# Optimization experiments

Measured on AMD Instinct MI355X. Metric: run time of the kernel, lower is better.

Reference implementation:

```python
import jax, jax.numpy as jnp
import numpy as np

SHAPES = ((496, 432), (248, 216), (124, 108))
NS = (40000, 20000, 8000)
T = 32
B = 4
EPS = 1e-3


def _bn(x, g, b, m, v):
    return (x - m) * (g / jnp.sqrt(v + EPS)) + b


def _vfe_scale(voxels, num_pts, w1, p1, w2, p2):
    # voxels: (N, T, 4); num_pts: (N,)
    Tp = voxels.shape[1]
    n = num_pts.astype(voxels.dtype)[:, None, None]
    m3 = voxels[:, :, :3].sum(axis=1, keepdims=True) / n
    m2 = voxels[:, :, :2].sum(axis=1, keepdims=True) / n
    feat = jnp.concatenate([voxels[:, :, :4], voxels[:, :, :3] - m3, voxels[:, :, :2] - m2], axis=-1)  # (N,T,9)
    mask = (jnp.arange(Tp)[None, :] < num_pts[:, None]).astype(voxels.dtype)[:, :, None]
    x = feat
    for w, (g, b_, rm, rv) in ((w1, p1), (w2, p2)):
        h = jax.nn.relu(_bn(jnp.einsum('ntc,cd->ntd', x, w), g, b_, rm, rv))  # (N,T,64)
        gmax = h.max(axis=1, keepdims=True)  # global max includes padded rows, as in torch source
        x = jnp.concatenate([h, jnp.broadcast_to(gmax, h.shape)], axis=-1) * mask  # (N,T,128)
    return x.max(axis=1)[:, :64]  # (N,64)


def _scatter_bev(vf, coords, h, w, batch_size):
    b = coords[:, 0]
    y = jnp.clip(coords[:, 2], 0, h - 1)
    x = jnp.clip(coords[:, 3], 0, w - 1)
    grid = jnp.zeros((batch_size, vf.shape[1], h, w), vf.dtype)
    return grid.at[b, :, y, x].set(vf)


def _fusion(x, w, g, b, m, v):
    y = jax.lax.conv_general_dilated(x, w, (1, 1), ((1, 1), (1, 1)),
                                     dimension_numbers=('NCHW', 'OIHW', 'NCHW'))
    y = _bn(y, g[None, :, None, None], b[None, :, None, None], m[None, :, None, None], v[None, :, None, None])
    return jax.nn.relu(y)


def setup_inputs() -> dict:
    key = jax.random.key(0)
    ks = jax.random.split(key, 32)
    inp = {}
    for s in range(3):
        h, w = SHAPES[s]
        inp[f'voxels_{s}'] = jax.random.normal(ks[s], (NS[s], T, 4), dtype=jnp.float32)
        inp[f'num_pts_{s}'] = jax.random.randint(ks[3 + s], (NS[s],), 1, T + 1, dtype=jnp.int32)
        b = jax.random.randint(ks[6 + s], (NS[s],), 0, B, dtype=jnp.int32)
        z = jnp.zeros((NS[s],), jnp.int32)
        y = jax.random.randint(ks[9 + s], (NS[s],), 0, h, dtype=jnp.int32)
        x = jax.random.randint(ks[12 + s], (NS[s],), 0, w, dtype=jnp.int32)
        inp[f'coords_{s}'] = jnp.stack([b, z, y, x], axis=1)
    # VFE params (stacked across the 3 scales; identical shapes per scale)
    inp['w1'] = jax.random.normal(ks[15], (3, 9, 64), dtype=jnp.float32) * 0.1
    inp['g1'] = jnp.ones((3, 64), jnp.float32) + 0.1 * jax.random.normal(ks[16], (3, 64))
    inp['b1'] = 0.05 * jax.random.normal(ks[17], (3, 64))
    inp['rm1'] = 0.05 * jax.random.normal(ks[18], (3, 64))
    inp['rv1'] = 0.5 + jnp.abs(jax.random.normal(ks[19], (3, 64)))
    inp['w2'] = jax.random.normal(ks[20], (3, 128, 64), dtype=jnp.float32) * 0.05
    inp['g2'] = jnp.ones((3, 64), jnp.float32) + 0.1 * jax.random.normal(ks[21], (3, 64))
    inp['b2'] = 0.05 * jax.random.normal(ks[22], (3, 64))
    inp['rm2'] = 0.05 * jax.random.normal(ks[23], (3, 64))
    inp['rv2'] = 0.5 + jnp.abs(jax.random.normal(ks[24], (3, 64)))
    # Fusion convs (2): Conv2d(128,64,3) + BN
    inp['fw'] = jax.random.normal(ks[25], (2, 64, 128, 3, 3), dtype=jnp.float32) * 0.03
    inp['fg'] = jnp.ones((2, 64), jnp.float32) + 0.1 * jax.random.normal(ks[26], (2, 64))
    inp['fb'] = 0.05 * jax.random.normal(ks[27], (2, 64))
    inp['fm'] = 0.05 * jax.random.normal(ks[28], (2, 64))
    inp['fv'] = 0.5 + jnp.abs(jax.random.normal(ks[29], (2, 64)))
    inp['batch_size'] = B
    return inp


def reference(voxels_0, voxels_1, voxels_2,
              w1, g1, b1, rm1, rv1, w2, g2, b2, rm2, rv2,
              fw, fg, fb, fm, fv,
              num_pts_0, num_pts_1, num_pts_2,
              coords_0, coords_1, coords_2, batch_size):
    voxels = (voxels_0, voxels_1, voxels_2)
    num_pts = (num_pts_0, num_pts_1, num_pts_2)
    coords = (coords_0, coords_1, coords_2)
    sf = []
    for s in range(3):
        vf = _vfe_scale(voxels[s], num_pts[s],
                        w1[s], (g1[s], b1[s], rm1[s], rv1[s]),
                        w2[s], (g2[s], b2[s], rm2[s], rv2[s]))
        h, w = SHAPES[s]
        sf.append(_scatter_bev(vf, coords[s], h, w, batch_size))
    # bottom-up fusion: scale2 -> scale1 -> scale0
    up = jax.image.resize(sf[2], sf[1].shape[:2] + SHAPES[1], method='bilinear')
    fused_1 = _fusion(jnp.concatenate([sf[1], up], axis=1), fw[1], fg[1], fb[1], fm[1], fv[1])
    up = jax.image.resize(fused_1, fused_1.shape[:2] + SHAPES[0], method='bilinear')
    fused_0 = _fusion(jnp.concatenate([sf[0], up], axis=1), fw[0], fg[0], fb[0], fm[0], fv[0])
    return fused_0  # spatial_features_2d: (B, 64, 496, 432)
```

## Files before the change

### kernel.cpp

```cpp
#include <hip/hip_runtime.h>

typedef unsigned short u16;
typedef short bf16x8 __attribute__((ext_vector_type(8)));
typedef float f32x4 __attribute__((ext_vector_type(4)));

#define EPSV 1e-3f

__device__ __forceinline__ float bf2f(u16 u) {
  union { unsigned int i; float f; } x; x.i = ((unsigned int)u) << 16; return x.f;
}
__device__ __forceinline__ u16 f2bf(float f) {
  union { float f; unsigned int i; } x; x.f = f;
  unsigned int r = x.i + 0x7fffu + ((x.i >> 16) & 1u);
  return (u16)(r >> 16);
}

#define WAVE_FENCE() do { __builtin_amdgcn_s_waitcnt(0); __builtin_amdgcn_wave_barrier(); } while (0)

__global__ void twt_kernel(const float* __restrict__ fw, u16* __restrict__ fwT) {
  int i = blockIdx.x * blockDim.x + threadIdx.x;
  if (i >= 2 * 9 * 64 * 128) return;
  int ci = i & 127;
  int r = i >> 7;
  int co = r & 63; r >>= 6;
  int kyx = r % 9;
  int set = r / 9;
  fwT[i] = f2bf(fw[(((set * 64 + co) * 128 + ci) * 9) + kyx]);
}

__global__ __launch_bounds__(256, 2) void vfe_mfma_kernel(
    const float* __restrict__ vox, const int* __restrict__ npts,
    const float* __restrict__ w1, const float* __restrict__ g1, const float* __restrict__ b1,
    const float* __restrict__ rm1, const float* __restrict__ rv1,
    const float* __restrict__ w2, const float* __restrict__ g2, const float* __restrict__ b2,
    const float* __restrict__ rm2, const float* __restrict__ rv2,
    float* __restrict__ vf, int N)
{
  struct PerWave {
    u16 X[32 * 72];
    u16 F[32 * 40];
    u16 G[64];
  };
  __shared__ __align__(16) union {
    struct { u16 W1T[64 * 40]; u16 W2T[64 * 136]; } w;
    PerWave r[4];
  } lds;

  const int tid = threadIdx.x;
  const int lane = tid & 63;
  const int wv = tid >> 6;
  const int m16 = lane & 15;
  const int q = lane >> 4;

  for (int i = tid; i < 64 * 40; i += 256) {
    int c = i / 40, k = i % 40;
    lds.w.W1T[i] = f2bf(k < 9 ? w1[k * 64 + c] : 0.f);
  }
  for (int i = tid; i < 64 * 136; i += 256) {
    int c = i / 136, j = i % 136;
    lds.w.W2T[i] = f2bf(j < 128 ? w2[j * 64 + c] : 0.f);
  }
  __syncthreads();

  bf16x8 bW1[4], bLo[4][2], bHi[4][2];
  float sc1[4], sh1[4], sc2[4], sh2[4];
#pragma unroll
  for (int nf = 0; nf < 4; ++nf) {
    int c = nf * 16 + m16;
    bW1[nf] = *(const bf16x8*)&lds.w.W1T[c * 40 + q * 8];
#pragma unroll
    for (int ks = 0; ks < 2; ++ks) {
      bLo[nf][ks] = *(const bf16x8*)&lds.w.W2T[c * 136 + ks * 32 + q * 8];
      bHi[nf][ks] = *(const bf16x8*)&lds.w.W2T[c * 136 + 64 + ks * 32 + q * 8];
    }
    float s1 = g1[c] * rsqrtf(rv1[c] + EPSV);
    sc1[nf] = s1; sh1[nf] = b1[c] - rm1[c] * s1;
    float s2 = g2[c] * rsqrtf(rv2[c] + EPSV);
    sc2[nf] = s2; sh2[nf] = b2[c] - rm2[c] * s2;
  }
  __syncthreads();

  u16* X = lds.r[wv].X;
  u16* F = lds.r[wv].F;
  u16* G = lds.r[wv].G;
  for (int i = lane; i < 640; i += 64) ((unsigned int*)F)[i] = 0u;

  const int wgid = blockIdx.x * 4 + wv;
  const int wstride = gridDim.x * 4;

  for (int v = wgid; v < N; v += wstride) {
    const int n = npts[v];
    float px = 0.f, py = 0.f, pz = 0.f, pw = 0.f;
    if (lane < 32) {
      float4 u = *(const float4*)(vox + ((size_t)v * 32 + lane) * 4);
      px = u.x; py = u.y; pz = u.z; pw = u.w;
    }
    float sx = px, sy = py, sz = pz;
#pragma unroll
    for (int off = 32; off >= 1; off >>= 1) {
      sx += __shfl_xor(sx, off);
      sy += __shfl_xor(sy, off);
      sz += __shfl_xor(sz, off);
    }
    float nf_ = (float)n;
    float mx = sx / nf_, my = sy / nf_, mz = sz / nf_;
    if (lane < 32) {
      float dx = px - mx, dy = py - my, dz = pz - mz;
      bf16x8 r0, r1;
      r0[0] = (short)f2bf(px); r0[1] = (short)f2bf(py);
      r0[2] = (short)f2bf(pz); r0[3] = (short)f2bf(pw);
      r0[4] = (short)f2bf(dx); r0[5] = (short)f2bf(dy);
      r0[6] = (short)f2bf(dz); r0[7] = (short)f2bf(dx);
      r1 = (bf16x8){0, 0, 0, 0, 0, 0, 0, 0};
      r1[0] = (short)f2bf(dy);
      *(bf16x8*)&F[lane * 40 + 0] = r0;
      *(bf16x8*)&F[lane * 40 + 8] = r1;
    }
    WAVE_FENCE();

    bf16x8 a1[2];
    a1[0] = *(const bf16x8*)&F[m16 * 40 + q * 8];
    a1[1] = *(const bf16x8*)&F[(16 + m16) * 40 + q * 8];
    f32x4 acc1[2][4];
#pragma unroll
    for (int mf = 0; mf < 2; ++mf)
#pragma unroll
      for (int nf = 0; nf < 4; ++nf) {
        acc1[mf][nf] = (f32x4){0.f, 0.f, 0.f, 0.f};
        acc1[mf][nf] = __builtin_amdgcn_mfma_f32_16x16x32_bf16(a1[mf], bW1[nf], acc1[mf][nf], 0, 0, 0);
      }

    float gmx[4] = {0.f, 0.f, 0.f, 0.f};
#pragma unroll
    for (int mf = 0; mf < 2; ++mf)
#pragma unroll
      for (int nf = 0; nf < 4; ++nf)
#pragma unroll
        for (int r = 0; r < 4; ++r) {
          float h = fmaxf(acc1[mf][nf][r] * sc1[nf] + sh1[nf], 0.f);
          gmx[nf] = fmaxf(gmx[nf], h);
          int t = mf * 16 + q * 4 + r;
          X[t * 72 + nf * 16 + m16] = f2bf(h);
        }
#pragma unroll
    for (int nf = 0; nf < 4; ++nf) {
      gmx[nf] = fmaxf(gmx[nf], __shfl_xor(gmx[nf], 16));
      gmx[nf] = fmaxf(gmx[nf], __shfl_xor(gmx[nf], 32));
    }
    if (q == 0) {
#pragma unroll
      for (int nf = 0; nf < 4; ++nf) G[nf * 16 + m16] = f2bf(gmx[nf]);
    }
    WAVE_FENCE();

    f32x4 ga[4];
#pragma unroll
    for (int nf = 0; nf < 4; ++nf) ga[nf] = (f32x4){0.f, 0.f, 0.f, 0.f};
#pragma unroll
    for (int ks = 0; ks < 2; ++ks) {
      bf16x8 ag = (bf16x8){0, 0, 0, 0, 0, 0, 0, 0};
      if (m16 == 0) ag = *(const bf16x8*)&G[ks * 32 + q * 8];
#pragma unroll
      for (int nf = 0; nf < 4; ++nf)
        ga[nf] = __builtin_amdgcn_mfma_f32_16x16x32_bf16(ag, bHi[nf][ks], ga[nf], 0, 0, 0);
    }
    float gt[4];
#pragma unroll
    for (int nf = 0; nf < 4; ++nf) {
      float s = ga[nf][0] + ga[nf][1] + ga[nf][2] + ga[nf][3];
      s += __shfl_xor(s, 16);
      s += __shfl_xor(s, 32);
      gt[nf] = s;
    }

    f32x4 acc2[2][4];
#pragma unroll
    for (int mf = 0; mf < 2; ++mf)
#pragma unroll
      for (int nf = 0; nf < 4; ++nf)
        acc2[mf][nf] = (f32x4){gt[nf], gt[nf], gt[nf], gt[nf]};
#pragma unroll
    for (int ks = 0; ks < 2; ++ks) {
      bf16x8 a2[2];
      a2[0] = *(const bf16x8*)&X[m16 * 72 + ks * 32 + q * 8];
      a2[1] = *(const bf16x8*)&X[(16 + m16) * 72 + ks * 32 + q * 8];
#pragma unroll
      for (int mf = 0; mf < 2; ++mf)
#pragma unroll
        for (int nf = 0; nf < 4; ++nf)
          acc2[mf][nf] = __builtin_amdgcn_mfma_f32_16x16x32_bf16(a2[mf], bLo[nf][ks], acc2[mf][nf], 0, 0, 0);
    }

    float vm[4] = {0.f, 0.f, 0.f, 0.f};
#pragma unroll
    for (int mf = 0; mf < 2; ++mf)
#pragma unroll
      for (int nf = 0; nf < 4; ++nf)
#pragma unroll
        for (int r = 0; r < 4; ++r) {
          int t = mf * 16 + q * 4 + r;
          float h2 = fmaxf(acc2[mf][nf][r] * sc2[nf] + sh2[nf], 0.f);
          if (t < n) vm[nf] = fmaxf(vm[nf], h2);
        }
#pragma unroll
    for (int nf = 0; nf < 4; ++nf) {
      vm[nf] = fmaxf(vm[nf], __shfl_xor(vm[nf], 16));
      vm[nf] = fmaxf(vm[nf], __shfl_xor(vm[nf], 32));
    }
    float outv = (q == 0) ? vm[0] : (q == 1) ? vm[1] : (q == 2) ? vm[2] : vm[3];
    vf[(size_t)v * 64 + q * 16 + m16] = outv;
    __builtin_amdgcn_wave_barrier();
  }
}

__global__ void winner_kernel(const int* __restrict__ coords, int* __restrict__ win,
                              int N, int H, int W) {
  int v = blockIdx.x * blockDim.x + threadIdx.x;
  if (v >= N) return;
  int b = coords[v * 4 + 0];
  int y = min(max(coords[v * 4 + 2], 0), H - 1);
  int x = min(max(coords[v * 4 + 3], 0), W - 1);
  atomicMax(&win[(b * H + y) * W + x], v);
}

__global__ void fill_kernel(const int* __restrict__ win, const float* __restrict__ vf,
                            u16* __restrict__ dst, int cells, int cstride) {
  int i = blockIdx.x * blockDim.x + threadIdx.x;
  if (i >= cells * 8) return;
  int cell = i >> 3, c8 = (i & 7) * 8;
  int wv = win[cell];
  bf16x8 o = (bf16x8){0, 0, 0, 0, 0, 0, 0, 0};
  if (wv >= 0) {
    const float* p = vf + (size_t)wv * 64 + c8;
    float4 v0 = *(const float4*)p;
    float4 v1 = *(const float4*)(p + 4);
    o[0] = (short)f2bf(v0.x); o[1] = (short)f2bf(v0.y);
    o[2] = (short)f2bf(v0.z); o[3] = (short)f2bf(v0.w);
    o[4] = (short)f2bf(v1.x); o[5] = (short)f2bf(v1.y);
    o[6] = (short)f2bf(v1.z); o[7] = (short)f2bf(v1.w);
  }
  *(bf16x8*)&dst[(size_t)cell * cstride + c8] = o;
}

__global__ void upsample_kernel(const u16* __restrict__ src, u16* __restrict__ dst,
                                int Hc, int Wc, int dstride, int doff, int total8) {
  int i = blockIdx.x * blockDim.x + threadIdx.x;
  if (i >= total8) return;
  int c8 = (i & 7) * 8;
  int px = i >> 3;
  int W2 = Wc * 2, H2 = Hc * 2;
  int x = px % W2; int t = px / W2; int y = t % H2; int n = t / H2;
  int ky = y >> 1, kx = x >> 1;
  int ya, yb, xa, xb; float wya, wxa;
  if ((y & 1) == 0) { ya = ky > 0 ? ky - 1 : 0; yb = ky; wya = 0.25f; }
  else              { ya = ky; yb = (ky + 1 < Hc) ? ky + 1 : Hc - 1; wya = 0.75f; }
  if ((x & 1) == 0) { xa = kx > 0 ? kx - 1 : 0; xb = kx; wxa = 0.25f; }
  else              { xa = kx; xb = (kx + 1 < Wc) ? kx + 1 : Wc - 1; wxa = 0.75f; }
  float wyb = 1.f - wya, wxb = 1.f - wxa;
  const u16* sp = src + c8;
  bf16x8 vaa = *(const bf16x8*)&sp[((size_t)(n * Hc + ya) * Wc + xa) * 64];
  bf16x8 vab = *(const bf16x8*)&sp[((size_t)(n * Hc + ya) * Wc + xb) * 64];
  bf16x8 vba = *(const bf16x8*)&sp[((size_t)(n * Hc + yb) * Wc + xa) * 64];
  bf16x8 vbb = *(const bf16x8*)&sp[((size_t)(n * Hc + yb) * Wc + xb) * 64];
  bf16x8 o;
#pragma unroll
  for (int j = 0; j < 8; ++j) {
    float v = wya * (wxa * bf2f((u16)vaa[j]) + wxb * bf2f((u16)vab[j])) +
              wyb * (wxa * bf2f((u16)vba[j]) + wxb * bf2f((u16)vbb[j]));
    o[j] = (short)f2bf(v);
  }
  *(bf16x8*)&dst[(size_t)px * dstride + doff + c8] = o;
}

template<int H, int W, bool NCHW_OUT>
__global__ __launch_bounds__(256, 2) void conv_kernel(
    const u16* __restrict__ in, const u16* __restrict__ wT,
    const float* __restrict__ fg, const float* __restrict__ fb,
    const float* __restrict__ fm, const float* __restrict__ fv,
    void* __restrict__ outv)
{
  constexpr int XT = 24, YT = 8;
  constexpr int XTILES = W / XT;
  constexpr int NPX = 10 * 26;
  __shared__ __align__(16) union {
    struct { char A[NPX * 128]; char B[2][8192]; } s;
    float T[4 * 64 * 33];
  } lds;

  const int tid = threadIdx.x;
  const int lane = tid & 63;
  const int wv = tid >> 6;
  const int m16 = lane & 15;
  const int q = lane >> 4;

  int bid = blockIdx.x;
  const int xt = bid % XTILES; bid /= XTILES;
  const int yt = bid % (H / YT);
  const int n = bid / (H / YT);
  const int x0 = xt * XT, y0 = yt * YT;

  int lin[3];
#pragma unroll
  for (int mf = 0; mf < 3; ++mf) {
    int m = mf * 16 + m16;
    int r = (m >= 24) ? 1 : 0;
    lin[mf] = (2 * wv + r) * 26 + (m - r * 24);
  }
  const int qb = q * 16;
  const int bsw = (m16 & 7) << 4;

  f32x4 acc[3][4];
#pragma unroll
  for (int mf = 0; mf < 3; ++mf)
#pragma unroll
    for (int nf = 0; nf < 4; ++nf)
      acc[mf][nf] = (f32x4){0.f, 0.f, 0.f, 0.f};

  for (int hf = 0; hf < 2; ++hf) {
    {
      const int slot = tid & 7;
      const int cis = slot * 8;
      const int pb = tid >> 3;
#pragma unroll
      for (int it = 0; it < 9; ++it) {
        int p = pb + it * 32;
        if (p < NPX) {
          int r = p / 26, xx = p - r * 26;
          int gy = y0 - 1 + r, gx = x0 - 1 + xx;
          uint4 v = make_uint4(0, 0, 0, 0);
          if (gy >= 0 && gy < H && gx >= 0 && gx < W)
            v = *(const uint4*)(in + ((size_t)((n * H + gy) * W + gx) * 128 + hf * 64 + cis));
          *(uint4*)(lds.s.A + p * 128 + ((slot << 4) ^ ((p & 7) << 4))) = v;
        }
      }
#pragma unroll
      for (int it = 0; it < 2; ++it) {
        int e = it * 256 + tid;
        int co = e >> 3, bs = e & 7;
        uint4 v = *(const uint4*)(wT + hf * 64 + co * 128 + bs * 8);
        *(uint4*)(lds.s.B[0] + co * 128 + ((bs << 4) ^ ((co & 7) << 4))) = v;
      }
    }
    __syncthreads();

#pragma unroll
    for (int kyx = 0; kyx < 9; ++kyx) {
      uint4 bv0, bv1;
      if (kyx < 8) {
        const u16* ws = wT + (kyx + 1) * 8192 + hf * 64;
        int co0 = tid >> 3, bs0 = tid & 7;
        bv0 = *(const uint4*)(ws + co0 * 128 + bs0 * 8);
        int e1 = 256 + tid;
        int co1 = e1 >> 3, bs1 = e1 & 7;
        bv1 = *(const uint4*)(ws + co1 * 128 + bs1 * 8);
      }
      const int tapofs = (kyx / 3) * 26 + (kyx % 3);
      const char* Bb = lds.s.B[kyx & 1];
#pragma unroll
      for (int cc = 0; cc < 2; ++cc) {
        const int o = cc * 64 + qb;
        bf16x8 b[4], a[3];
#pragma unroll
        for (int nf = 0; nf < 4; ++nf)
          b[nf] = *(const bf16x8*)(Bb + nf * 2048 + m16 * 128 + (o ^ bsw));
#pragma unroll
        for (int mf = 0; mf < 3; ++mf) {
          int p = lin[mf] + tapofs;
          a[mf] = *(const bf16x8*)(lds.s.A + p * 128 + (o ^ ((p & 7) << 4)));
        }
#pragma unroll
        for (int mf = 0; mf < 3; ++mf)
#pragma unroll
          for (int nf = 0; nf < 4; ++nf)
            acc[mf][nf] = __builtin_amdgcn_mfma_f32_16x16x32_bf16(a[mf], b[nf], acc[mf][nf], 0, 0, 0);
      }
      if (kyx < 8) {
        char* Bw = lds.s.B[(kyx + 1) & 1];
        int co0 = tid >> 3, bs0 = tid & 7;
        *(uint4*)(Bw + co0 * 128 + ((bs0 << 4) ^ ((co0 & 7) << 4))) = bv0;
        int e1 = 256 + tid;
        int co1 = e1 >> 3, bs1 = e1 & 7;
        *(uint4*)(Bw + co1 * 128 + ((bs1 << 4) ^ ((co1 & 7) << 4))) = bv1;
      }
      __syncthreads();
    }
  }

  float sc[4], sh[4];
#pragma unroll
  for (int nf = 0; nf < 4; ++nf) {
    int co = nf * 16 + m16;
    float s = fg[co] * rsqrtf(fv[co] + EPSV);
    sc[nf] = s;
    sh[nf] = fb[co] - fm[co] * s;
  }

  if (!NCHW_OUT) {
    u16* out = (u16*)outv;
#pragma unroll
    for (int mf = 0; mf < 3; ++mf)
#pragma unroll
      for (int nf = 0; nf < 4; ++nf)
#pragma unroll
        for (int r = 0; r < 4; ++r) {
          int mpos = mf * 16 + q * 4 + r;
          int rr = (mpos >= 24) ? 1 : 0;
          int px = mpos - rr * 24;
          int y = y0 + wv * 2 + rr;
          int x = x0 + px;
          int co = nf * 16 + m16;
          float v = fmaxf(acc[mf][nf][r] * sc[nf] + sh[nf], 0.f);
          out[((size_t)(n * H + y) * W + x) * 64 + co] = f2bf(v);
        }
  } else {
    __syncthreads();
    float* out = (float*)outv;
    float* T = &lds.T[wv * 64 * 33];
#pragma unroll
    for (int rr = 0; rr < 2; ++rr) {
#pragma unroll
      for (int mf = 0; mf < 3; ++mf)
#pragma unroll
        for (int nf = 0; nf < 4; ++nf)
#pragma unroll
          for (int r = 0; r < 4; ++r) {
            int mpos = mf * 16 + q * 4 + r;
            if ((mpos >= 24 ? 1 : 0) == rr) {
              int px = mpos - rr * 24;
              int co = nf * 16 + m16;
              T[co * 33 + px] = fmaxf(acc[mf][nf][r] * sc[nf] + sh[nf], 0.f);
            }
          }
      WAVE_FENCE();
      const int px = lane & 31, co2 = lane >> 5;
      const int y = y0 + wv * 2 + rr;
      int x = x0 + px;
#pragma unroll 4
      for (int it = 0; it < 32; ++it) {
        int co = it * 2 + co2;
        float v = T[co * 33 + px];
        if (px < 24) out[((size_t)(n * 64 + co) * H + y) * W + x] = v;
      }
      WAVE_FENCE();
    }
  }
}

extern "C" void kernel_launch(void* const* d_in, const int* in_sizes, int n_in,
                              void* d_out, int out_size, void* d_ws, size_t ws_size,
                              hipStream_t stream) {
  int I_vox[3], I_np[3], I_co[3];
  int I_w1, I_g1, I_b1, I_rm1, I_rv1, I_w2, I_g2, I_b2, I_rm2, I_rv2;
  int I_fw, I_fg, I_fb, I_fm, I_fv;
  if (in_sizes[1] == 40000) {
    I_vox[0] = 0; I_np[0] = 1; I_co[0] = 2;
    I_vox[1] = 3; I_np[1] = 4; I_co[1] = 5;
    I_vox[2] = 6; I_np[2] = 7; I_co[2] = 8;
    I_w1 = 9; I_g1 = 10; I_b1 = 11; I_rm1 = 12; I_rv1 = 13;
    I_w2 = 14; I_g2 = 15; I_b2 = 16; I_rm2 = 17; I_rv2 = 18;
    I_fw = 19; I_fg = 20; I_fb = 21; I_fm = 22; I_fv = 23;
  } else {
    I_vox[0] = 0; I_vox[1] = 1; I_vox[2] = 2;
    I_w1 = 3; I_g1 = 4; I_b1 = 5; I_rm1 = 6; I_rv1 = 7;
    I_w2 = 8; I_g2 = 9; I_b2 = 10; I_rm2 = 11; I_rv2 = 12;
    I_fw = 13; I_fg = 14; I_fb = 15; I_fm = 16; I_fv = 17;
    I_np[0] = 18; I_np[1] = 19; I_np[2] = 20;
    I_co[0] = 21; I_co[1] = 22; I_co[2] = 23;
  }

  const int HS[3] = {496, 248, 124};
  const int WS[3] = {432, 216, 108};
  int Nv[3];
  for (int s = 0; s < 3; ++s) Nv[s] = in_sizes[I_np[s]];

  char* wsp = (char*)d_ws;
  size_t off = 0;
  auto take = [&](size_t bytes) -> void* {
    void* p = wsp + off;
    off = (off + bytes + 255) & ~(size_t)255;
    return p;
  };
  float* vf[3]; int* win[3];
  for (int s = 0; s < 3; ++s) vf[s] = (float*)take((size_t)Nv[s] * 64 * 4);
  int cells[3];
  for (int s = 0; s < 3; ++s) {
    cells[s] = 4 * HS[s] * WS[s];
    win[s] = (int*)take((size_t)cells[s] * 4);
  }
  u16* buf0 = (u16*)take((size_t)cells[0] * 128 * 2);
  u16* buf1 = (u16*)take((size_t)cells[1] * 128 * 2);
  u16* g2b  = (u16*)take((size_t)cells[2] * 64 * 2);
  u16* fus1 = (u16*)take((size_t)cells[1] * 64 * 2);
  u16* fwT  = (u16*)take((size_t)2 * 9 * 64 * 128 * 2);

  const float* W1 = (const float*)d_in[I_w1];
  const float* G1 = (const float*)d_in[I_g1];
  const float* B1 = (const float*)d_in[I_b1];
  const float* RM1 = (const float*)d_in[I_rm1];
  const float* RV1 = (const float*)d_in[I_rv1];
  const float* W2 = (const float*)d_in[I_w2];
  const float* G2 = (const float*)d_in[I_g2];
  const float* B2 = (const float*)d_in[I_b2];
  const float* RM2 = (const float*)d_in[I_rm2];
  const float* RV2 = (const float*)d_in[I_rv2];
  const float* FW = (const float*)d_in[I_fw];
  const float* FG = (const float*)d_in[I_fg];
  const float* FB = (const float*)d_in[I_fb];
  const float* FM = (const float*)d_in[I_fm];
  const float* FV = (const float*)d_in[I_fv];

  for (int s = 0; s < 3; ++s)
    hipMemsetAsync(win[s], 0xFF, (size_t)cells[s] * 4, stream);

  twt_kernel<<<(2 * 9 * 64 * 128 + 255) / 256, 256, 0, stream>>>(FW, fwT);

  for (int s = 0; s < 3; ++s) {
    int blocks = (Nv[s] + 3) / 4;
    if (blocks > 1024) blocks = 1024;
    vfe_mfma_kernel<<<blocks, 256, 0, stream>>>(
        (const float*)d_in[I_vox[s]], (const int*)d_in[I_np[s]],
        W1 + s * 9 * 64, G1 + s * 64, B1 + s * 64, RM1 + s * 64, RV1 + s * 64,
        W2 + s * 128 * 64, G2 + s * 64, B2 + s * 64, RM2 + s * 64, RV2 + s * 64,
        vf[s], Nv[s]);
  }
  for (int s = 0; s < 3; ++s) {
    winner_kernel<<<(Nv[s] + 255) / 256, 256, 0, stream>>>(
        (const int*)d_in[I_co[s]], win[s], Nv[s], HS[s], WS[s]);
  }
  fill_kernel<<<(cells[0] * 8 + 255) / 256, 256, 0, stream>>>(win[0], vf[0], buf0, cells[0], 128);
  fill_kernel<<<(cells[1] * 8 + 255) / 256, 256, 0, stream>>>(win[1], vf[1], buf1, cells[1], 128);
  fill_kernel<<<(cells[2] * 8 + 255) / 256, 256, 0, stream>>>(win[2], vf[2], g2b, cells[2], 64);

  {
    int total8 = cells[1] * 8;
    upsample_kernel<<<(total8 + 255) / 256, 256, 0, stream>>>(g2b, buf1, 124, 108, 128, 64, total8);
  }
  conv_kernel<248, 216, false><<<4 * (248 / 8) * (216 / 24), 256, 0, stream>>>(
      buf1, fwT + 9 * 64 * 128, FG + 64, FB + 64, FM + 64, FV + 64, fus1);
  {
    int total8 = cells[0] * 8;
    upsample_kernel<<<(total8 + 255) / 256, 256, 0, stream>>>(fus1, buf0, 248, 216, 128, 64, total8);
  }
  conv_kernel<496, 432, true><<<4 * (496 / 8) * (432 / 24), 256, 0, stream>>>(
      buf0, fwT, FG, FB, FM, FV, (float*)d_out);
}
```

Baseline: 831.6 us.

## Widen conv tile to 32 columns with four M fragments and edge masking

The conv tile width grows from 24 to 32 pixels, so each wave computes four 16-row MFMA fragments instead of three. Each B-weight fragment load is then reused across more A fragments, and the halo overhead per output pixel shrinks. Widths that are not multiples of 32 (216, 432) need partial tiles, which wastes some compute on masked columns and adds bounds checks. LDS use and accumulator register pressure also rise.

```diff
diff --git a/kernel.cpp b/kernel.cpp
--- a/kernel.cpp
+++ b/kernel.cpp
@@ -279,9 +279,9 @@
     const float* __restrict__ fm, const float* __restrict__ fv,
     void* __restrict__ outv)
 {
-  constexpr int XT = 24, YT = 8;
-  constexpr int XTILES = W / XT;
-  constexpr int NPX = 10 * 26;
+  constexpr int XT = 32, YT = 8;
+  constexpr int XTILES = (W + XT - 1) / XT;
+  constexpr int NPX = 10 * 34;
   __shared__ __align__(16) union {
     struct { char A[NPX * 128]; char B[2][8192]; } s;
     float T[4 * 64 * 33];
@@ -299,19 +299,18 @@
   const int n = bid / (H / YT);
   const int x0 = xt * XT, y0 = yt * YT;
 
-  int lin[3];
-#pragma unroll
-  for (int mf = 0; mf < 3; ++mf) {
+  int lin[4];
+#pragma unroll
+  for (int mf = 0; mf < 4; ++mf) {
     int m = mf * 16 + m16;
-    int r = (m >= 24) ? 1 : 0;
-    lin[mf] = (2 * wv + r) * 26 + (m - r * 24);
+    lin[mf] = (2 * wv + (m >> 5)) * 34 + (m & 31);
   }
   const int qb = q * 16;
   const int bsw = (m16 & 7) << 4;
 
-  f32x4 acc[3][4];
-#pragma unroll
-  for (int mf = 0; mf < 3; ++mf)
+  f32x4 acc[4][4];
+#pragma unroll
+  for (int mf = 0; mf < 4; ++mf)
 #pragma unroll
     for (int nf = 0; nf < 4; ++nf)
       acc[mf][nf] = (f32x4){0.f, 0.f, 0.f, 0.f};
@@ -322,10 +321,10 @@
       const int cis = slot * 8;
       const int pb = tid >> 3;
 #pragma unroll
-      for (int it = 0; it < 9; ++it) {
+      for (int it = 0; it < 11; ++it) {
         int p = pb + it * 32;
         if (p < NPX) {
-          int r = p / 26, xx = p - r * 26;
+          int r = p / 34, xx = p - r * 34;
           int gy = y0 - 1 + r, gx = x0 - 1 + xx;
           uint4 v = make_uint4(0, 0, 0, 0);
           if (gy >= 0 && gy < H && gx >= 0 && gx < W)
@@ -354,22 +353,22 @@
         int co1 = e1 >> 3, bs1 = e1 & 7;
         bv1 = *(const uint4*)(ws + co1 * 128 + bs1 * 8);
       }
-      const int tapofs = (kyx / 3) * 26 + (kyx % 3);
+      const int tapofs = (kyx / 3) * 34 + (kyx % 3);
       const char* Bb = lds.s.B[kyx & 1];
 #pragma unroll
       for (int cc = 0; cc < 2; ++cc) {
         const int o = cc * 64 + qb;
-        bf16x8 b[4], a[3];
+        bf16x8 b[4], a[4];
 #pragma unroll
         for (int nf = 0; nf < 4; ++nf)
           b[nf] = *(const bf16x8*)(Bb + nf * 2048 + m16 * 128 + (o ^ bsw));
 #pragma unroll
-        for (int mf = 0; mf < 3; ++mf) {
+        for (int mf = 0; mf < 4; ++mf) {
           int p = lin[mf] + tapofs;
           a[mf] = *(const bf16x8*)(lds.s.A + p * 128 + (o ^ ((p & 7) << 4)));
         }
 #pragma unroll
-        for (int mf = 0; mf < 3; ++mf)
+        for (int mf = 0; mf < 4; ++mf)
 #pragma unroll
           for (int nf = 0; nf < 4; ++nf)
             acc[mf][nf] = __builtin_amdgcn_mfma_f32_16x16x32_bf16(a[mf], b[nf], acc[mf][nf], 0, 0, 0);
@@ -398,48 +397,46 @@
   if (!NCHW_OUT) {
     u16* out = (u16*)outv;
 #pragma unroll
-    for (int mf = 0; mf < 3; ++mf)
+    for (int mf = 0; mf < 4; ++mf) {
+      int y = y0 + wv * 2 + (mf >> 1);
 #pragma unroll
       for (int nf = 0; nf < 4; ++nf)
 #pragma unroll
         for (int r = 0; r < 4; ++r) {
-          int mpos = mf * 16 + q * 4 + r;
-          int rr = (mpos >= 24) ? 1 : 0;
-          int px = mpos - rr * 24;
-          int y = y0 + wv * 2 + rr;
+          int px = (mf & 1) * 16 + q * 4 + r;
           int x = x0 + px;
-          int co = nf * 16 + m16;
-          float v = fmaxf(acc[mf][nf][r] * sc[nf] + sh[nf], 0.f);
-          out[((size_t)(n * H + y) * W + x) * 64 + co] = f2bf(v);
+          if (x < W) {
+            int co = nf * 16 + m16;
+            float v = fmaxf(acc[mf][nf][r] * sc[nf] + sh[nf], 0.f);
+            out[((size_t)(n * H + y) * W + x) * 64 + co] = f2bf(v);
+          }
         }
+    }
   } else {
     __syncthreads();
     float* out = (float*)outv;
     float* T = &lds.T[wv * 64 * 33];
 #pragma unroll
-    for (int rr = 0; rr < 2; ++rr) {
-#pragma unroll
-      for (int mf = 0; mf < 3; ++mf)
+    for (int yr = 0; yr < 2; ++yr) {
+#pragma unroll
+      for (int xc = 0; xc < 2; ++xc)
 #pragma unroll
         for (int nf = 0; nf < 4; ++nf)
 #pragma unroll
           for (int r = 0; r < 4; ++r) {
-            int mpos = mf * 16 + q * 4 + r;
-            if ((mpos >= 24 ? 1 : 0) == rr) {
-              int px = mpos - rr * 24;
-              int co = nf * 16 + m16;
-              T[co * 33 + px] = fmaxf(acc[mf][nf][r] * sc[nf] + sh[nf], 0.f);
-            }
+            int px = xc * 16 + q * 4 + r;
+            int co = nf * 16 + m16;
+            T[co * 33 + px] = fmaxf(acc[yr * 2 + xc][nf][r] * sc[nf] + sh[nf], 0.f);
           }
       WAVE_FENCE();
       const int px = lane & 31, co2 = lane >> 5;
-      const int y = y0 + wv * 2 + rr;
+      const int y = y0 + wv * 2 + yr;
       int x = x0 + px;
 #pragma unroll 4
       for (int it = 0; it < 32; ++it) {
         int co = it * 2 + co2;
         float v = T[co * 33 + px];
-        if (px < 24) out[((size_t)(n * 64 + co) * H + y) * W + x] = v;
+        if (x < W) out[((size_t)(n * 64 + co) * H + y) * W + x] = v;
       }
       WAVE_FENCE();
     }
@@ -535,12 +532,12 @@
     int total8 = cells[1] * 8;
     upsample_kernel<<<(total8 + 255) / 256, 256, 0, stream>>>(g2b, buf1, 124, 108, 128, 64, total8);
   }
-  conv_kernel<248, 216, false><<<4 * (248 / 8) * (216 / 24), 256, 0, stream>>>(
+  conv_kernel<248, 216, false><<<4 * (248 / 8) * 7, 256, 0, stream>>>(
       buf1, fwT + 9 * 64 * 128, FG + 64, FB + 64, FM + 64, FV + 64, fus1);
   {
     int total8 = cells[0] * 8;
     upsample_kernel<<<(total8 + 255) / 256, 256, 0, stream>>>(fus1, buf0, 248, 216, 128, 64, total8);
   }
-  conv_kernel<496, 432, true><<<4 * (496 / 8) * (432 / 24), 256, 0, stream>>>(
+  conv_kernel<496, 432, true><<<4 * (496 / 8) * 14, 256, 0, stream>>>(
       buf0, fwT, FG, FB, FM, FV, (float*)d_out);
 }
```

Result: faster. 764.9 us (-8.0%).
